# Kernel tuning notes

Measured on AMD Instinct MI355X. Metric: run time of the kernel, lower is better.

Reference implementation:

```python
import jax, jax.numpy as jnp
import numpy as np

B, N, DIM = 8, 512, 512
HEADS, HD = 8, 64          # head_dim = dim // num_heads
E_ATT = 24                 # num_attn_experts, top-k = HEADS
E_FFD, K_FFD = 16, 2       # num_ffd_experts, top-k = ffd_heads
HID = 1024                 # int(dim*mlp_ratio) // ffd_heads = 2048 // 2
TASKS = 9
SWITCH_W, Z_W = 0.01, 0.001
SCALE = HD ** -0.5


def layer_norm(x, g, b, eps=1e-5):
    m = x.mean(-1, keepdims=True)
    v = ((x - m) ** 2).mean(-1, keepdims=True)
    return (x - m) * jax.lax.rsqrt(v + eps) * g + b


def top_k_gating(xf, w_gate, k, n_experts):
    # xf: [T, C], w_gate: [C, E]  (eval mode: no noise)
    logits = xf @ w_gate                                      # [T, E]
    probs = jax.nn.softmax(logits, axis=-1)
    vals, idx = jax.lax.top_k(probs, k)                       # [T, k]
    denom = jax.lax.stop_gradient(vals.sum(-1, keepdims=True) + 1e-6)
    gates = vals / denom                                      # renormalized top-k gates
    one_hot = jax.nn.one_hot(idx, n_experts, dtype=probs.dtype)  # [T, k, E]
    freqs = jax.lax.stop_gradient(one_hot.sum((0, 1)))        # tokens per expert [E]
    p_sum = probs.sum(0)
    switch = n_experts * jnp.sum((p_sum / p_sum.sum()) * (freqs / freqs.sum()))
    z = jnp.mean(jax.nn.logsumexp(logits, axis=-1) ** 2)
    loss = SWITCH_W * switch + Z_W * z
    return gates, one_hot, loss


def _forward(x, task_bh, norm1_g, norm1_b, gate_att, wq, wo_att, kv_w, kv_b,
             norm2_g, norm2_b, gate_mlp, wi, bi, wo_mlp, bo):
    Bs, Ns, C = x.shape
    T = Bs * Ns
    # ---- MoE task attention (MoA-style: experts produce query heads) ----
    x1 = layer_norm(x, norm1_g, norm1_b).reshape(T, C)
    gates, oh, loss1 = top_k_gating(x1, gate_att[task_bh], HEADS, E_ATT)
    # map: per-slot expert query projection (not gate-weighted)
    q_all = jnp.einsum('tc,ech->teh', x1, wq)                 # [T, E, hd]
    q = jnp.einsum('teh,tke->tkh', q_all, oh)                 # [T, H, hd]
    q = q.reshape(Bs, Ns, HEADS, HD)
    kv = x1 @ kv_w + kv_b                                     # shared single-head k,v
    k_, v_ = jnp.split(kv.reshape(Bs, Ns, 2 * HD), 2, axis=-1)
    attn = jnp.einsum('bihd,bjd->bhij', q, k_) * SCALE
    attn = jax.nn.softmax(attn, axis=-1)
    o = jnp.einsum('bhij,bjd->bihd', attn, v_).reshape(T, HEADS, HD)
    # reduce: gate-weighted per-expert output projection
    comb = jnp.einsum('tkd,tk,tke->ted', o, gates, oh)        # [T, E, hd]
    y = jnp.einsum('ted,edc->tc', comb, wo_att).reshape(Bs, Ns, C)
    x = x + y
    # ---- MoE task MLP ----
    x2 = layer_norm(x, norm2_g, norm2_b).reshape(T, C)
    gates2, oh2, loss2 = top_k_gating(x2, gate_mlp[task_bh], K_FFD, E_FFD)
    g_dense = jnp.einsum('tk,tke->te', gates2, oh2)           # sparse gates densified [T,E]
    h = jax.nn.gelu(jnp.einsum('tc,ech->teh', x2, wi) + bi, approximate=False)
    y2 = jnp.einsum('teh,te,ehc->tc', h, g_dense, wo_mlp) + g_dense @ bo
    x = x + y2.reshape(Bs, Ns, C)
    return x, loss1 + loss2


def setup_inputs() -> dict:
    key = jax.random.key(0)
    ks = jax.random.split(key, 8)
    s = 0.02
    return {
        'x': jax.random.normal(ks[0], (B, N, DIM), jnp.float32),
        'task_bh': 3,
        'norm1_g': jnp.ones((DIM,), jnp.float32),
        'norm1_b': jnp.zeros((DIM,), jnp.float32),
        'gate_att': jax.random.normal(ks[1], (TASKS, DIM, E_ATT), jnp.float32) * s,
        'wq': jax.random.normal(ks[2], (E_ATT, DIM, HD), jnp.float32) * s,
        'wo_att': jax.random.normal(ks[3], (E_ATT, HD, DIM), jnp.float32) * s,
        'kv_w': jax.random.normal(ks[4], (DIM, 2 * HD), jnp.float32) * s,
        'kv_b': jnp.zeros((2 * HD,), jnp.float32),
        'norm2_g': jnp.ones((DIM,), jnp.float32),
        'norm2_b': jnp.zeros((DIM,), jnp.float32),
        'gate_mlp': jax.random.normal(ks[5], (TASKS, DIM, E_FFD), jnp.float32) * s,
        'wi': jax.random.normal(ks[6], (E_FFD, DIM, HID), jnp.float32) * s,
        'bi': jnp.zeros((E_FFD, HID), jnp.float32),
        'wo_mlp': jax.random.normal(ks[7], (E_FFD, HID, DIM), jnp.float32) * s,
        'bo': jnp.zeros((E_FFD, DIM), jnp.float32),
    }


def reference(x, task_bh, norm1_g, norm1_b, gate_att, wq, wo_att, kv_w, kv_b,
              norm2_g, norm2_b, gate_mlp, wi, bi, wo_mlp, bo):
    return _forward(x, task_bh, norm1_g, norm1_b, gate_att, wq, wo_att, kv_w, kv_b,
                    norm2_g, norm2_b, gate_mlp, wi, bi, wo_mlp, bo)
```

## Files before the change

### kernel.cpp

```cpp
#include <hip/hip_runtime.h>
#include <math.h>

namespace {

constexpr int T   = 4096;
constexpr int C   = 512;
constexpr int NB  = 8;
constexpr int NS  = 512;
constexpr int HD  = 64;
constexpr int KA  = 8;
constexpr int EA  = 24;
constexpr int EF  = 16;
constexpr int KF  = 2;
constexpr int HID = 1024;

typedef __attribute__((ext_vector_type(8))) short bf16x8;
typedef __attribute__((ext_vector_type(4))) float f32x4;

__device__ inline unsigned short f2bf(float f) {
  unsigned u = __float_as_uint(f);
  return (unsigned short)((u + 0x7FFFu + ((u >> 16) & 1u)) >> 16);
}
__device__ inline float bf2f(unsigned short u) {
  return __uint_as_float((unsigned)u << 16);
}

template <int E, int TS>
__device__ inline bool tile_from_counts(const int* counts, int tile, int& e_out, int& t0_out) {
  int e = 0;
  for (; e < E; e++) {
    int nt = (counts[e] + TS - 1) / TS;
    if (tile < nt) break;
    tile -= nt;
  }
  e_out = e; t0_out = tile * TS;
  return e < E;
}

template <int E, int K, bool RESID>
__global__ __launch_bounds__(1024) void ln_gate_kernel(
    const float* __restrict__ in, const unsigned short* __restrict__ yslot,
    float* __restrict__ resid_out,
    const float* __restrict__ g, const float* __restrict__ b,
    const float* __restrict__ gate_all, const int* __restrict__ task,
    unsigned short* __restrict__ outb,
    float* __restrict__ probs, float* __restrict__ lse_out,
    float* __restrict__ gates, int* __restrict__ idxs) {
  constexpr int TPB = 16;
  constexpr int XSS = 516;
  int tid = threadIdx.x, lane = tid & 63, wv = tid >> 6;
  int tb = blockIdx.x * TPB;
  __shared__ float xs[TPB][XSS];
  __shared__ float lp[2][TPB][E];
  __shared__ __align__(16) float Wt[E][XSS];
  const float* W = gate_all + (size_t)task[0] * C * E;
  for (int i = tid; i < C * E; i += 1024) {
    int c = i / E, e = i - c * E;
    Wt[e][c] = W[i];
  }
  int c0 = lane * 8;
  const float4 g0 = *(const float4*)&g[c0], g1 = *(const float4*)&g[c0 + 4];
  const float4 b0 = *(const float4*)&b[c0], b1 = *(const float4*)&b[c0 + 4];
  {
    int tt = wv;
    int t = tb + tt;
    const float* row = in + (size_t)t * C + c0;
    float4 v0 = *(const float4*)&row[0];
    float4 v1 = *(const float4*)&row[4];
    if (RESID) {
      #pragma unroll
      for (int k = 0; k < KA; k++) {
        uint4 u = *(const uint4*)&yslot[((size_t)t * KA + k) * C + c0];
        const unsigned short* us = (const unsigned short*)&u;
        v0.x += bf2f(us[0]); v0.y += bf2f(us[1]); v0.z += bf2f(us[2]); v0.w += bf2f(us[3]);
        v1.x += bf2f(us[4]); v1.y += bf2f(us[5]); v1.z += bf2f(us[6]); v1.w += bf2f(us[7]);
      }
      *(float4*)&resid_out[(size_t)t * C + c0]     = v0;
      *(float4*)&resid_out[(size_t)t * C + c0 + 4] = v1;
    }
    float s = (v0.x + v0.y) + (v0.z + v0.w) + (v1.x + v1.y) + (v1.z + v1.w);
    #pragma unroll
    for (int m = 1; m < 64; m <<= 1) s += __shfl_xor(s, m);
    float mean = s * (1.f / C);
    float d[8] = {v0.x - mean, v0.y - mean, v0.z - mean, v0.w - mean,
                  v1.x - mean, v1.y - mean, v1.z - mean, v1.w - mean};
    float vv = 0.f;
    #pragma unroll
    for (int j = 0; j < 8; j++) vv += d[j] * d[j];
    #pragma unroll
    for (int m = 1; m < 64; m <<= 1) vv += __shfl_xor(vv, m);
    float r = rsqrtf(vv * (1.f / C) + 1e-5f);
    float o[8];
    o[0] = d[0] * r * g0.x + b0.x; o[1] = d[1] * r * g0.y + b0.y;
    o[2] = d[2] * r * g0.z + b0.z; o[3] = d[3] * r * g0.w + b0.w;
    o[4] = d[4] * r * g1.x + b1.x; o[5] = d[5] * r * g1.y + b1.y;
    o[6] = d[6] * r * g1.z + b1.z; o[7] = d[7] * r * g1.w + b1.w;
    *(ushort4*)&outb[(size_t)t * C + c0] =
        make_ushort4(f2bf(o[0]), f2bf(o[1]), f2bf(o[2]), f2bf(o[3]));
    *(ushort4*)&outb[(size_t)t * C + c0 + 4] =
        make_ushort4(f2bf(o[4]), f2bf(o[5]), f2bf(o[6]), f2bf(o[7]));
    #pragma unroll
    for (int j = 0; j < 8; j++) xs[tt][c0 + j] = o[j];
  }
  __syncthreads();
  if (tid < TPB * E * 2) {
    int half = tid / (TPB * E);
    int rem = tid - half * (TPB * E);
    int e = rem % E, tt = rem / E;
    int cb = half * (C / 2);
    float a0 = 0.f, a1 = 0.f, a2 = 0.f, a3 = 0.f;
    float a4 = 0.f, a5 = 0.f, a6 = 0.f, a7 = 0.f;
    #pragma unroll 4
    for (int c = cb; c < cb + C / 2; c += 8) {
      const float4 xv0 = *(const float4*)&xs[tt][c];
      const float4 xv1 = *(const float4*)&xs[tt][c + 4];
      const float4 wv0 = *(const float4*)&Wt[e][c];
      const float4 wv1 = *(const float4*)&Wt[e][c + 4];
      a0 += xv0.x * wv0.x; a1 += xv0.y * wv0.y;
      a2 += xv0.z * wv0.z; a3 += xv0.w * wv0.w;
      a4 += xv1.x * wv1.x; a5 += xv1.y * wv1.y;
      a6 += xv1.z * wv1.z; a7 += xv1.w * wv1.w;
    }
    lp[half][tt][e] = ((a0 + a1) + (a2 + a3)) + ((a4 + a5) + (a6 + a7));
  }
  __syncthreads();
  {
    int tt = wv;
    int t = tb + tt;
    float lgv = (lane < E) ? (lp[0][tt][lane] + lp[1][tt][lane]) : -3.0e38f;
    float mx = lgv;
    #pragma unroll
    for (int m = 1; m < 64; m <<= 1) mx = fmaxf(mx, __shfl_xor(mx, m));
    float pe = (lane < E) ? expf(lgv - mx) : 0.f;
    float sum = pe;
    #pragma unroll
    for (int m = 1; m < 64; m <<= 1) sum += __shfl_xor(sum, m);
    float inv = 1.f / sum;
    float prob = pe * inv;
    if (lane < E) probs[(size_t)t * E + lane] = prob;
    if (lane == 0) lse_out[t] = mx + logf(sum);
    float pv = (lane < E) ? prob : -1.f;
    float gsum = 0.f, myv = 0.f; int myi = 0;
    for (int k = 0; k < K; k++) {
      float bv = pv; int bi_ = lane;
      #pragma unroll
      for (int m = 1; m < 64; m <<= 1) {
        float ov = __shfl_xor(bv, m); int oi = __shfl_xor(bi_, m);
        if (ov > bv || (ov == bv && oi < bi_)) { bv = ov; bi_ = oi; }
      }
      gsum += bv;
      if (lane == k) { myv = bv; myi = bi_; }
      if (lane == bi_) pv = -1.f;
    }
    if (lane < K) {
      float ginv = 1.f / (gsum + 1e-6f);
      gates[(size_t)t * K + lane] = myv * ginv;
      idxs[(size_t)t * K + lane]  = myi;
    }
  }
}

template <int E>
__global__ __launch_bounds__(512) void bucket_kernel(const int* __restrict__ idx, int nslots,
                                                     int stride, int* counts, int* bucket) {
  __shared__ int lcount[E];
  __shared__ int lbase[E];
  int tid = threadIdx.x;
  if (tid < E) lcount[tid] = 0;
  __syncthreads();
  int s = blockIdx.x * 512 + tid;
  int e = 0, lpos = 0;
  bool valid = (s < nslots);
  if (valid) {
    e = idx[s];
    lpos = atomicAdd(&lcount[e], 1);
  }
  __syncthreads();
  if (tid < E) lbase[tid] = lcount[tid] ? atomicAdd(&counts[tid], lcount[tid]) : 0;
  __syncthreads();
  if (valid) bucket[(size_t)e * stride + lbase[e] + lpos] = s;
}

__global__ __launch_bounds__(256) void tcvt_all(
    const float* __restrict__ wq, const float* __restrict__ wo_a,
    const float* __restrict__ wi, const float* __restrict__ wo_m,
    const float* __restrict__ kvw,
    unsigned short* __restrict__ wqt, unsigned short* __restrict__ woat,
    unsigned short* __restrict__ wit, unsigned short* __restrict__ womt,
    unsigned short* __restrict__ kvwt) {
  int bid = blockIdx.x;
  const float* src; unsigned short* dst; int K, N, nx, rem;
  if (bid < 768)        { src = wq;   dst = wqt;  K = 512;  N = 64;   nx = 2;  rem = bid; }
  else if (bid < 1536)  { src = wo_a; dst = woat; K = 64;   N = 512;  nx = 16; rem = bid - 768; }
  else if (bid < 9728)  { src = wi;   dst = wit;  K = 512;  N = 1024; nx = 32; rem = bid - 1536; }
  else if (bid < 17920) { src = wo_m; dst = womt; K = 1024; N = 512;  nx = 16; rem = bid - 9728; }
  else                  { src = kvw;  dst = kvwt; K = 512;  N = 128;  nx = 4;  rem = bid - 17920; }
  int per = nx * (K / 32);
  int e = rem / per, r2 = rem % per;
  int kt = (r2 / nx) * 32, nt = (r2 % nx) * 32;
  __shared__ float tile[32][33];
  int tid = threadIdx.x;
  const float* S = src + (size_t)e * K * N;
  for (int i = tid; i < 32 * 32; i += 256) {
    int r = i >> 5, c = i & 31;
    tile[r][c] = S[(size_t)(kt + r) * N + nt + c];
  }
  __syncthreads();
  unsigned short* D = dst + (size_t)e * K * N;
  for (int i = tid; i < 32 * 8; i += 256) {
    int n = i >> 3, k4 = (i & 7) * 4;
    ushort4 v;
    v.x = f2bf(tile[k4 + 0][n]); v.y = f2bf(tile[k4 + 1][n]);
    v.z = f2bf(tile[k4 + 2][n]); v.w = f2bf(tile[k4 + 3][n]);
    *(ushort4*)&D[(size_t)(nt + n) * K + kt + k4] = v;
  }
}

__global__ __launch_bounds__(256) void qgemm_mfma(
    const unsigned short* __restrict__ xb, const unsigned short* __restrict__ wqt,
    const int* __restrict__ bucket, const int* __restrict__ counts,
    unsigned short* __restrict__ qb) {
  __shared__ int se, st0;
  int tid = threadIdx.x;
  if (tid == 0) {
    int e, t0;
    bool ok = tile_from_counts<EA, 64>(counts, blockIdx.y, e, t0);
    se = ok ? e : -1; st0 = t0;
  }
  __syncthreads();
  if (se < 0) return;
  int e = se, t0 = st0;
  int cnt = counts[e];
  __shared__ int slots[64];
  __shared__ __align__(16) unsigned short Xb[64][72];
  __shared__ __align__(16) unsigned short Wb[64][72];
  if (tid < 64) {
    int ii = t0 + tid;
    slots[tid] = (ii < cnt) ? bucket[(size_t)e * (T * KA) + ii] : -1;
  }
  __syncthreads();
  int lane = tid & 63, w = tid >> 6;
  int lr = lane & 15, lk = (lane >> 4) * 8, rowq = (lane >> 4) * 4;
  f32x4 acc[4] = {};
  for (int kc = 0; kc < C; kc += 64) {
    __syncthreads();
    #pragma unroll
    for (int it = 0; it < 2; ++it) {
      int i = it * 256 + tid;
      int r = i >> 3, c8 = (i & 7) * 8;
      int s = slots[r];
      uint4 v = make_uint4(0u, 0u, 0u, 0u);
      if (s >= 0) v = *(const uint4*)&xb[(size_t)(s >> 3) * C + kc + c8];
      *(uint4*)&Xb[r][c8] = v;
    }
    #pragma unroll
    for (int it = 0; it < 2; ++it) {
      int i = it * 256 + tid;
      int r = i >> 3, c8 = (i & 7) * 8;
      *(uint4*)&Wb[r][c8] = *(const uint4*)&wqt[((size_t)e * HD + r) * C + kc + c8];
    }
    __syncthreads();
    #pragma unroll
    for (int kk = 0; kk < 64; kk += 32) {
      bf16x8 a = *(const bf16x8*)&Wb[w * 16 + lr][kk + lk];
      #pragma unroll
      for (int mf = 0; mf < 4; mf++) {
        bf16x8 b = *(const bf16x8*)&Xb[mf * 16 + lr][kk + lk];
        acc[mf] = __builtin_amdgcn_mfma_f32_16x16x32_bf16(a, b, acc[mf], 0, 0, 0);
      }
    }
  }
  #pragma unroll
  for (int mf = 0; mf < 4; mf++) {
    int s = slots[mf * 16 + lr];
    if (s < 0) continue;
    ushort4 v = make_ushort4(f2bf(0.125f * acc[mf][0]), f2bf(0.125f * acc[mf][1]),
                             f2bf(0.125f * acc[mf][2]), f2bf(0.125f * acc[mf][3]));
    *(ushort4*)&qb[(size_t)s * HD + w * 16 + rowq] = v;
  }
}

__global__ __launch_bounds__(256) void kv_mfma(
    const unsigned short* __restrict__ xb, const unsigned short* __restrict__ kvwt,
    const float* __restrict__ kvb, unsigned short* __restrict__ Kb,
    unsigned short* __restrict__ Vt) {
  int t0 = blockIdx.x * 16;
  int tid = threadIdx.x;
  __shared__ __align__(16) unsigned short Xs[16][72];
  __shared__ __align__(16) unsigned short Ws[128][72];
  int lane = tid & 63, w = tid >> 6;
  int lr = lane & 15, lk = (lane >> 4) * 8, rowq = (lane >> 4) * 4;
  f32x4 acc[2] = {};
  for (int kc = 0; kc < C; kc += 64) {
    __syncthreads();
    if (tid < 128) {
      int r = tid >> 3, c8 = (tid & 7) * 8;
      *(uint4*)&Xs[r][c8] = *(const uint4*)&xb[(size_t)(t0 + r) * C + kc + c8];
    }
    #pragma unroll
    for (int it = 0; it < 4; ++it) {
      int i = it * 256 + tid;
      int r = i >> 3, c8 = (i & 7) * 8;
      *(uint4*)&Ws[r][c8] = *(const uint4*)&kvwt[(size_t)r * C + kc + c8];
    }
    __syncthreads();
    #pragma unroll
    for (int kk = 0; kk < 64; kk += 32) {
      bf16x8 xf = *(const bf16x8*)&Xs[lr][kk + lk];
      #pragma unroll
      for (int cf = 0; cf < 2; cf++) {
        bf16x8 wf = *(const bf16x8*)&Ws[w * 32 + cf * 16 + lr][kk + lk];
        acc[cf] = __builtin_amdgcn_mfma_f32_16x16x32_bf16(wf, xf, acc[cf], 0, 0, 0);
      }
    }
  }
  int t = t0 + lr;
  int bb = t >> 9, n = t & (NS - 1);
  #pragma unroll
  for (int cf = 0; cf < 2; cf++) {
    #pragma unroll
    for (int r2 = 0; r2 < 4; r2++) {
      int c = w * 32 + cf * 16 + rowq + r2;
      float v = acc[cf][r2] + kvb[c];
      if (c < HD) Kb[(size_t)t * HD + c] = f2bf(v);
      else        Vt[((size_t)bb * HD + (c - HD)) * NS + n] = f2bf(v);
    }
  }
}

__global__ __launch_bounds__(256) void attn_mfma(
    const unsigned short* __restrict__ qb, const unsigned short* __restrict__ Kb,
    const unsigned short* __restrict__ Vt, unsigned short* __restrict__ ob) {
  int qt = blockIdx.x, h = blockIdx.y, b = blockIdx.z;
  int tid = threadIdx.x;
  __shared__ __align__(16) unsigned short Qs[64][72];
  __shared__ __align__(16) unsigned short Ks[64][72];
  __shared__ __align__(16) unsigned short Vs[64][72];
  __shared__ __align__(16) unsigned short Ps[64][72];
  int i0 = qt * 64;
  #pragma unroll
  for (int it = 0; it < 2; ++it) {
    int i = it * 256 + tid;
    int r = i >> 3, c8 = (i & 7) * 8;
    *(uint4*)&Qs[r][c8] = *(const uint4*)&qb[(((size_t)(b * NS + i0 + r)) * KA + h) * HD + c8];
  }
  int lane = tid & 63, w = tid >> 6;
  int lr = lane & 15, lk = (lane >> 4) * 8, rowq = (lane >> 4) * 4;
  f32x4 acc_o[4] = {};
  float m_run = -3.0e38f, l_run = 0.f;
  for (int jt = 0; jt < NS / 64; ++jt) {
    __syncthreads();
    #pragma unroll
    for (int it = 0; it < 2; ++it) {
      int i = it * 256 + tid;
      int r = i >> 3, c8 = (i & 7) * 8;
      *(uint4*)&Ks[r][c8] = *(const uint4*)&Kb[((size_t)(b * NS + jt * 64 + r)) * HD + c8];
      *(uint4*)&Vs[r][c8] = *(const uint4*)&Vt[((size_t)b * HD + r) * NS + jt * 64 + c8];
    }
    __syncthreads();
    f32x4 acc_s[4] = {};
    #pragma unroll
    for (int kk = 0; kk < 64; kk += 32) {
      bf16x8 qf = *(const bf16x8*)&Qs[w * 16 + lr][kk + lk];
      #pragma unroll
      for (int kf = 0; kf < 4; kf++) {
        bf16x8 kr = *(const bf16x8*)&Ks[kf * 16 + lr][kk + lk];
        acc_s[kf] = __builtin_amdgcn_mfma_f32_16x16x32_bf16(kr, qf, acc_s[kf], 0, 0, 0);
      }
    }
    float pmax = acc_s[0][0];
    #pragma unroll
    for (int kf = 0; kf < 4; kf++)
      #pragma unroll
      for (int r = 0; r < 4; r++) pmax = fmaxf(pmax, acc_s[kf][r]);
    pmax = fmaxf(pmax, __shfl_xor(pmax, 16));
    pmax = fmaxf(pmax, __shfl_xor(pmax, 32));
    float m_new = fmaxf(m_run, pmax);
    float scl = expf(m_run - m_new);
    float rs = 0.f;
    #pragma unroll
    for (int kf = 0; kf < 4; kf++)
      #pragma unroll
      for (int r = 0; r < 4; r++) {
        float pv = expf(acc_s[kf][r] - m_new);
        rs += pv;
        Ps[w * 16 + lr][kf * 16 + rowq + r] = f2bf(pv);
      }
    rs += __shfl_xor(rs, 16);
    rs += __shfl_xor(rs, 32);
    l_run = l_run * scl + rs;
    m_run = m_new;
    __syncthreads();
    #pragma unroll
    for (int df = 0; df < 4; df++) {
      acc_o[df][0] *= scl; acc_o[df][1] *= scl;
      acc_o[df][2] *= scl; acc_o[df][3] *= scl;
    }
    #pragma unroll
    for (int kk = 0; kk < 64; kk += 32) {
      bf16x8 pf = *(const bf16x8*)&Ps[w * 16 + lr][kk + lk];
      #pragma unroll
      for (int df = 0; df < 4; df++) {
        bf16x8 vf = *(const bf16x8*)&Vs[df * 16 + lr][kk + lk];
        acc_o[df] = __builtin_amdgcn_mfma_f32_16x16x32_bf16(vf, pf, acc_o[df], 0, 0, 0);
      }
    }
  }
  float inv = 1.f / l_run;
  int token = b * NS + i0 + w * 16 + lr;
  #pragma unroll
  for (int df = 0; df < 4; df++) {
    ushort4 v = make_ushort4(f2bf(acc_o[df][0] * inv), f2bf(acc_o[df][1] * inv),
                             f2bf(acc_o[df][2] * inv), f2bf(acc_o[df][3] * inv));
    *(ushort4*)&ob[((size_t)token * KA + h) * HD + df * 16 + rowq] = v;
  }
}

__global__ __launch_bounds__(256) void oproj_mfma(
    const unsigned short* __restrict__ ob, const unsigned short* __restrict__ wot,
    const float* __restrict__ gates, const int* __restrict__ bucket,
    const int* __restrict__ counts, unsigned short* __restrict__ y_slot) {
  __shared__ int se, st0;
  int tid = threadIdx.x;
  if (tid == 0) {
    int e, t0;
    bool ok = tile_from_counts<EA, 128>(counts, blockIdx.y, e, t0);
    se = ok ? e : -1; st0 = t0;
  }
  __syncthreads();
  if (se < 0) return;
  int e = se, t0 = st0;
  int c0 = blockIdx.x * 128;
  int cnt = counts[e];
  __shared__ int slots[128];
  __shared__ float gs[128];
  __shared__ __align__(16) unsigned short Xb[128][72];
  __shared__ __align__(16) unsigned short Wb[128][72];
  if (tid < 128) {
    int ii = t0 + tid;
    int s = (ii < cnt) ? bucket[(size_t)e * (T * KA) + ii] : -1;
    slots[tid] = s;
    gs[tid] = (s >= 0) ? gates[s] : 0.f;
  }
  __syncthreads();
  #pragma unroll
  for (int it = 0; it < 4; ++it) {
    int i = it * 256 + tid;
    int r = i >> 3, c8 = (i & 7) * 8;
    int s = slots[r];
    uint4 vo = make_uint4(0u, 0u, 0u, 0u);
    if (s >= 0) {
      float g = gs[r];
      uint4 u = *(const uint4*)&ob[(size_t)s * HD + c8];
      const unsigned short* us = (const unsigned short*)&u;
      unsigned short* vs = (unsigned short*)&vo;
      #pragma unroll
      for (int k = 0; k < 8; k++) vs[k] = f2bf(g * bf2f(us[k]));
    }
    *(uint4*)&Xb[r][c8] = vo;
  }
  #pragma unroll
  for (int it = 0; it < 4; ++it) {
    int i = it * 256 + tid;
    int r = i >> 3, c8 = (i & 7) * 8;
    *(uint4*)&Wb[r][c8] = *(const uint4*)&wot[((size_t)e * C + c0 + r) * HD + c8];
  }
  __syncthreads();
  int lane = tid & 63, wid = tid >> 6;
  int wr = wid & 1, wc = wid >> 1;
  int lr = lane & 15, lk = (lane >> 4) * 8, rowq = (lane >> 4) * 4;
  f32x4 acc[4][4] = {};
  #pragma unroll
  for (int kk = 0; kk < 64; kk += 32) {
    bf16x8 a[4], b[4];
    #pragma unroll
    for (int nf = 0; nf < 4; nf++) a[nf] = *(const bf16x8*)&Wb[wc * 64 + nf * 16 + lr][kk + lk];
    #pragma unroll
    for (int mf = 0; mf < 4; mf++) b[mf] = *(const bf16x8*)&Xb[wr * 64 + mf * 16 + lr][kk + lk];
    #pragma unroll
    for (int nf = 0; nf < 4; nf++)
      #pragma unroll
      for (int mf = 0; mf < 4; mf++)
        acc[nf][mf] = __builtin_amdgcn_mfma_f32_16x16x32_bf16(a[nf], b[mf], acc[nf][mf], 0, 0, 0);
  }
  #pragma unroll
  for (int mf = 0; mf < 4; mf++) {
    int si = wr * 64 + mf * 16 + lr;
    int s = slots[si];
    if (s < 0) continue;
    size_t base = (size_t)s * C + c0 + wc * 64;
    #pragma unroll
    for (int nf = 0; nf < 4; nf++) {
      ushort4 v = make_ushort4(f2bf(acc[nf][mf][0]), f2bf(acc[nf][mf][1]),
                               f2bf(acc[nf][mf][2]), f2bf(acc[nf][mf][3]));
      *(ushort4*)&y_slot[base + nf * 16 + rowq] = v;
    }
  }
}

__global__ __launch_bounds__(256) void mlp1_mfma(
    const unsigned short* __restrict__ xb, const unsigned short* __restrict__ wit,
    const float* __restrict__ bi, const int* __restrict__ bucket,
    const int* __restrict__ counts, unsigned short* __restrict__ h) {
  __shared__ int se, st0;
  int tid = threadIdx.x;
  if (tid == 0) {
    int e, t0;
    bool ok = tile_from_counts<EF, 64>(counts, blockIdx.y, e, t0);
    se = ok ? e : -1; st0 = t0;
  }
  __syncthreads();
  if (se < 0) return;
  int e = se, t0 = st0;
  int j0 = blockIdx.x * 64;
  int cnt = counts[e];
  __shared__ int slots[64];
  __shared__ __align__(16) unsigned short Xb[64][72];
  __shared__ __align__(16) unsigned short Wb[64][72];
  if (tid < 64) {
    int ii = t0 + tid;
    slots[tid] = (ii < cnt) ? bucket[(size_t)e * (T * KF) + ii] : -1;
  }
  __syncthreads();
  int lane = tid & 63, w = tid >> 6;
  int lr = lane & 15, lk = (lane >> 4) * 8, rowq = (lane >> 4) * 4;
  f32x4 acc[4] = {};
  for (int kc = 0; kc < C; kc += 64) {
    __syncthreads();
    #pragma unroll
    for (int it = 0; it < 2; ++it) {
      int i = it * 256 + tid;
      int r = i >> 3, c8 = (i & 7) * 8;
      int s = slots[r];
      uint4 v = make_uint4(0u, 0u, 0u, 0u);
      if (s >= 0) v = *(const uint4*)&xb[(size_t)(s >> 1) * C + kc + c8];
      *(uint4*)&Xb[r][c8] = v;
    }
    #pragma unroll
    for (int it = 0; it < 2; ++it) {
      int i = it * 256 + tid;
      int r = i >> 3, c8 = (i & 7) * 8;
      *(uint4*)&Wb[r][c8] = *(const uint4*)&wit[((size_t)e * HID + j0 + r) * C + kc + c8];
    }
    __syncthreads();
    #pragma unroll
    for (int kk = 0; kk < 64; kk += 32) {
      bf16x8 a = *(const bf16x8*)&Wb[w * 16 + lr][kk + lk];
      #pragma unroll
      for (int mf = 0; mf < 4; mf++) {
        bf16x8 b = *(const bf16x8*)&Xb[mf * 16 + lr][kk + lk];
        acc[mf] = __builtin_amdgcn_mfma_f32_16x16x32_bf16(a, b, acc[mf], 0, 0, 0);
      }
    }
  }
  #pragma unroll
  for (int mf = 0; mf < 4; mf++) {
    int s = slots[mf * 16 + lr];
    if (s < 0) continue;
    int j = j0 + w * 16 + rowq;
    const float4 b4 = *(const float4*)&bi[(size_t)e * HID + j];
    float v0 = acc[mf][0] + b4.x, v1 = acc[mf][1] + b4.y;
    float v2 = acc[mf][2] + b4.z, v3 = acc[mf][3] + b4.w;
    v0 = 0.5f * v0 * (1.f + erff(v0 * 0.70710678118654752f));
    v1 = 0.5f * v1 * (1.f + erff(v1 * 0.70710678118654752f));
    v2 = 0.5f * v2 * (1.f + erff(v2 * 0.70710678118654752f));
    v3 = 0.5f * v3 * (1.f + erff(v3 * 0.70710678118654752f));
    *(ushort4*)&h[(size_t)s * HID + j] = make_ushort4(f2bf(v0), f2bf(v1), f2bf(v2), f2bf(v3));
  }
}

__global__ __launch_bounds__(256) void mlp2_mfma(
    const unsigned short* __restrict__ h, const unsigned short* __restrict__ wot,
    const float* __restrict__ bo, const float* __restrict__ gates2,
    const int* __restrict__ bucket, const int* __restrict__ counts,
    unsigned short* __restrict__ y2) {
  __shared__ int se, st0;
  int tid = threadIdx.x;
  if (tid == 0) {
    int e, t0;
    bool ok = tile_from_counts<EF, 64>(counts, blockIdx.y, e, t0);
    se = ok ? e : -1; st0 = t0;
  }
  __syncthreads();
  if (se < 0) return;
  int e = se, t0 = st0;
  int c0 = blockIdx.x * 64;
  int cnt = counts[e];
  __shared__ int slots[64];
  __shared__ __align__(16) unsigned short Xb[64][72];
  __shared__ __align__(16) unsigned short Wb[64][72];
  if (tid < 64) {
    int ii = t0 + tid;
    slots[tid] = (ii < cnt) ? bucket[(size_t)e * (T * KF) + ii] : -1;
  }
  __syncthreads();
  int lane = tid & 63, w = tid >> 6;
  int lr = lane & 15, lk = (lane >> 4) * 8, rowq = (lane >> 4) * 4;
  f32x4 acc[4] = {};
  for (int kc = 0; kc < HID; kc += 64) {
    __syncthreads();
    #pragma unroll
    for (int it = 0; it < 2; ++it) {
      int i = it * 256 + tid;
      int r = i >> 3, c8 = (i & 7) * 8;
      int s = slots[r];
      uint4 v = make_uint4(0u, 0u, 0u, 0u);
      if (s >= 0) v = *(const uint4*)&h[(size_t)s * HID + kc + c8];
      *(uint4*)&Xb[r][c8] = v;
    }
    #pragma unroll
    for (int it = 0; it < 2; ++it) {
      int i = it * 256 + tid;
      int r = i >> 3, c8 = (i & 7) * 8;
      *(uint4*)&Wb[r][c8] = *(const uint4*)&wot[((size_t)e * C + c0 + r) * HID + kc + c8];
    }
    __syncthreads();
    #pragma unroll
    for (int kk = 0; kk < 64; kk += 32) {
      bf16x8 a = *(const bf16x8*)&Wb[w * 16 + lr][kk + lk];
      #pragma unroll
      for (int mf = 0; mf < 4; mf++) {
        bf16x8 b = *(const bf16x8*)&Xb[mf * 16 + lr][kk + lk];
        acc[mf] = __builtin_amdgcn_mfma_f32_16x16x32_bf16(a, b, acc[mf], 0, 0, 0);
      }
    }
  }
  #pragma unroll
  for (int mf = 0; mf < 4; mf++) {
    int s = slots[mf * 16 + lr];
    if (s < 0) continue;
    float g = gates2[s];
    int cc = c0 + w * 16 + rowq;
    const float4 b4 = *(const float4*)&bo[(size_t)e * C + cc];
    ushort4 v = make_ushort4(f2bf(g * (acc[mf][0] + b4.x)),
                             f2bf(g * (acc[mf][1] + b4.y)),
                             f2bf(g * (acc[mf][2] + b4.z)),
                             f2bf(g * (acc[mf][3] + b4.w)));
    *(ushort4*)&y2[(size_t)s * C + cc] = v;
  }
}

__global__ void final_kernel(const unsigned short* __restrict__ y2, float* __restrict__ xout) {
  int t = blockIdx.x, tid = threadIdx.x;
  int c = tid * 2;
  unsigned u0 = *(const unsigned*)&y2[(size_t)(t * 2) * C + c];
  unsigned u1 = *(const unsigned*)&y2[(size_t)(t * 2 + 1) * C + c];
  xout[(size_t)t * C + c]     += bf2f((unsigned short)(u0 & 0xFFFF)) + bf2f((unsigned short)(u1 & 0xFFFF));
  xout[(size_t)t * C + c + 1] += bf2f((unsigned short)(u0 >> 16)) + bf2f((unsigned short)(u1 >> 16));
}

__global__ __launch_bounds__(256) void reduce_gating_all(
    const float* __restrict__ probs1, const float* __restrict__ lse1,
    const int* __restrict__ idx1,
    const float* __restrict__ probs2, const float* __restrict__ lse2,
    const int* __restrict__ idx2, float* __restrict__ accum) {
  constexpr int TPB = 64, TPW = 16;
  int which = blockIdx.y;
  int E = which ? EF : EA;
  int K = which ? KF : KA;
  const float* probs = which ? probs2 : probs1;
  const float* lse   = which ? lse2 : lse1;
  const int* idxs    = which ? idx2 : idx1;
  float* psum = accum + (which ? 49 : 0);
  float* freq = accum + (which ? 65 : 24);
  float* zsum = accum + (which ? 81 : 48);
  int tid = threadIdx.x, lane = tid & 63, wv = tid >> 6;
  int t0 = blockIdx.x * TPB + wv * TPW;
  float ps = 0.f, fr = 0.f;
  if (lane < E) {
    for (int i = 0; i < TPW; i++) {
      int t = t0 + i;
      ps += probs[(size_t)t * E + lane];
      for (int k = 0; k < K; k++)
        fr += (idxs[(size_t)t * K + k] == lane) ? 1.f : 0.f;
    }
  }
  float z = 0.f;
  for (int i = lane; i < TPW; i += 64) {
    float l = lse[t0 + i];
    z += l * l;
  }
  #pragma unroll
  for (int m = 1; m < 64; m <<= 1) z += __shfl_xor(z, m);
  __shared__ float sps[4][EA];
  __shared__ float sfr[4][EA];
  __shared__ float sz[4];
  if (lane < E) { sps[wv][lane] = ps; sfr[wv][lane] = fr; }
  if (lane == 0) sz[wv] = z;
  __syncthreads();
  if (tid < E) {
    atomicAdd(&psum[tid], sps[0][tid] + sps[1][tid] + sps[2][tid] + sps[3][tid]);
    atomicAdd(&freq[tid], sfr[0][tid] + sfr[1][tid] + sfr[2][tid] + sfr[3][tid]);
  }
  if (tid == 255) atomicAdd(zsum, sz[0] + sz[1] + sz[2] + sz[3]);
}

__global__ void loss_kernel(const float* __restrict__ acc, float* __restrict__ out) {
  const float* p1 = acc;      const float* f1 = acc + 24; float z1 = acc[48];
  const float* p2 = acc + 49; const float* f2 = acc + 65; float z2 = acc[81];
  float sp1 = 0.f, sf1 = 0.f;
  for (int e = 0; e < 24; e++) { sp1 += p1[e]; sf1 += f1[e]; }
  float sw1 = 0.f;
  for (int e = 0; e < 24; e++) sw1 += (p1[e] / sp1) * (f1[e] / sf1);
  sw1 *= 24.f;
  float sp2 = 0.f, sf2 = 0.f;
  for (int e = 0; e < 16; e++) { sp2 += p2[e]; sf2 += f2[e]; }
  float sw2 = 0.f;
  for (int e = 0; e < 16; e++) sw2 += (p2[e] / sp2) * (f2[e] / sf2);
  sw2 *= 16.f;
  out[0] = 0.01f * sw1 + 0.001f * (z1 / T) + 0.01f * sw2 + 0.001f * (z2 / T);
}

}

extern "C" void kernel_launch(void* const* d_in, const int* in_sizes, int n_in,
                              void* d_out, int out_size, void* d_ws, size_t ws_size,
                              hipStream_t stream) {
  const float* x      = (const float*)d_in[0];
  const int*   task   = (const int*)d_in[1];
  const float* n1g    = (const float*)d_in[2];
  const float* n1b    = (const float*)d_in[3];
  const float* gate_a = (const float*)d_in[4];
  const float* wq     = (const float*)d_in[5];
  const float* wo_a   = (const float*)d_in[6];
  const float* kvw    = (const float*)d_in[7];
  const float* kvb    = (const float*)d_in[8];
  const float* n2g    = (const float*)d_in[9];
  const float* n2b    = (const float*)d_in[10];
  const float* gate_m = (const float*)d_in[11];
  const float* wi     = (const float*)d_in[12];
  const float* bi     = (const float*)d_in[13];
  const float* wo_m   = (const float*)d_in[14];
  const float* bo     = (const float*)d_in[15];
  float* out = (float*)d_out;

  char* p = (char*)d_ws;
  unsigned short* x1b = (unsigned short*)p; p += (size_t)T * C * 2;
  unsigned short* qb = (unsigned short*)p;  p += (size_t)T * KA * HD * 2;
  unsigned short* ob = (unsigned short*)p;  p += (size_t)T * KA * HD * 2;
  unsigned short* Kb = (unsigned short*)p;  p += (size_t)T * HD * 2;
  unsigned short* Vt = (unsigned short*)p;  p += (size_t)T * HD * 2;
  char* un = p;                      p += (size_t)T * KA * C * 2;
  unsigned short* y_slot  = (unsigned short*)un;
  unsigned short* h       = (unsigned short*)un;
  unsigned short* y2_slot = (unsigned short*)(un + (size_t)T * KF * HID * 2);
  unsigned short* wqt = (unsigned short*)p;  p += (size_t)EA * C * HD * 2;
  unsigned short* woat = (unsigned short*)p; p += (size_t)EA * HD * C * 2;
  unsigned short* wit = (unsigned short*)p;  p += (size_t)EF * C * HID * 2;
  unsigned short* womt = (unsigned short*)p; p += (size_t)EF * HID * C * 2;
  unsigned short* kvwt = (unsigned short*)p; p += (size_t)(2 * HD) * C * 2;
  float* probs1 = (float*)p;         p += (size_t)T * EA * 4;
  float* lse1 = (float*)p;           p += (size_t)T * 4;
  float* gates1 = (float*)p;         p += (size_t)T * KA * 4;
  int* idx1 = (int*)p;               p += (size_t)T * KA * 4;
  float* probs2 = (float*)p;         p += (size_t)T * EF * 4;
  float* lse2 = (float*)p;           p += (size_t)T * 4;
  float* gates2 = (float*)p;         p += (size_t)T * KF * 4;
  int* idx2 = (int*)p;               p += (size_t)T * KF * 4;
  int* bucket_a = (int*)p;           p += (size_t)EA * (T * KA) * 4;
  int* bucket_f = (int*)p;           p += (size_t)EF * (T * KF) * 4;
  int* counts_a = (int*)p;           p += 32 * 4;
  int* counts_f = (int*)p;           p += 32 * 4;
  float* accum = (float*)p;          p += 128 * 4;

  hipMemsetAsync(counts_a, 0, (32 + 32 + 128) * 4, stream);

  tcvt_all<<<17984, 256, 0, stream>>>(wq, wo_a, wi, wo_m, kvw, wqt, woat, wit, womt, kvwt);

  ln_gate_kernel<EA, KA, false><<<T / 16, 1024, 0, stream>>>(
      x, y_slot, out, n1g, n1b, gate_a, task, x1b, probs1, lse1, gates1, idx1);
  bucket_kernel<EA><<<(T * KA + 511) / 512, 512, 0, stream>>>(idx1, T * KA, T * KA,
                                                              counts_a, bucket_a);
  qgemm_mfma<<<dim3(1, 536), 256, 0, stream>>>(x1b, wqt, bucket_a, counts_a, qb);
  kv_mfma<<<T / 16, 256, 0, stream>>>(x1b, kvwt, kvb, Kb, Vt);
  attn_mfma<<<dim3(NS / 64, KA, NB), 256, 0, stream>>>(qb, Kb, Vt, ob);
  oproj_mfma<<<dim3(4, 280), 256, 0, stream>>>(ob, woat, gates1, bucket_a, counts_a, y_slot);
  ln_gate_kernel<EF, KF, true><<<T / 16, 1024, 0, stream>>>(
      x, y_slot, out, n2g, n2b, gate_m, task, x1b, probs2, lse2, gates2, idx2);
  bucket_kernel<EF><<<(T * KF + 511) / 512, 512, 0, stream>>>(idx2, T * KF, T * KF,
                                                              counts_f, bucket_f);
  mlp1_mfma<<<dim3(16, 144), 256, 0, stream>>>(x1b, wit, bi, bucket_f, counts_f, h);
  mlp2_mfma<<<dim3(8, 144), 256, 0, stream>>>(h, womt, bo, gates2, bucket_f, counts_f, y2_slot);
  final_kernel<<<T, 256, 0, stream>>>(y2_slot, out);
  reduce_gating_all<<<dim3(T / 64, 2), 256, 0, stream>>>(probs1, lse1, idx1,
                                                         probs2, lse2, idx2, accum);
  loss_kernel<<<1, 1, 0, stream>>>(accum, out + (size_t)T * C);
}
```

Baseline: 229.4 us.

## Merge Q and KV projections into one launch, retile weight convert and attention

Combines the routed Q projection and the shared KV projection into a single kernel whose grid covers both kinds of tile, saving one launch and letting the two overlap. The weight convert-transpose kernel now uses 64x64 tiles with float4 loads, giving four times fewer blocks, though its stores become scalar 2-byte writes. Attention blocks drop to 128 threads covering 32 query rows each, which doubles the block count to raise occupancy but loads each K/V tile twice as often overall.

```diff
diff --git a/kernel.cpp b/kernel.cpp
--- a/kernel.cpp
+++ b/kernel.cpp
@@ -190,157 +190,153 @@
     unsigned short* __restrict__ kvwt) {
   int bid = blockIdx.x;
   const float* src; unsigned short* dst; int K, N, nx, rem;
-  if (bid < 768)        { src = wq;   dst = wqt;  K = 512;  N = 64;   nx = 2;  rem = bid; }
-  else if (bid < 1536)  { src = wo_a; dst = woat; K = 64;   N = 512;  nx = 16; rem = bid - 768; }
-  else if (bid < 9728)  { src = wi;   dst = wit;  K = 512;  N = 1024; nx = 32; rem = bid - 1536; }
-  else if (bid < 17920) { src = wo_m; dst = womt; K = 1024; N = 512;  nx = 16; rem = bid - 9728; }
-  else                  { src = kvw;  dst = kvwt; K = 512;  N = 128;  nx = 4;  rem = bid - 17920; }
-  int per = nx * (K / 32);
+  if (bid < 192)       { src = wq;   dst = wqt;  K = 512;  N = 64;   nx = 1;  rem = bid; }
+  else if (bid < 384)  { src = wo_a; dst = woat; K = 64;   N = 512;  nx = 8;  rem = bid - 192; }
+  else if (bid < 2432) { src = wi;   dst = wit;  K = 512;  N = 1024; nx = 16; rem = bid - 384; }
+  else if (bid < 4480) { src = wo_m; dst = womt; K = 1024; N = 512;  nx = 8;  rem = bid - 2432; }
+  else                 { src = kvw;  dst = kvwt; K = 512;  N = 128;  nx = 2;  rem = bid - 4480; }
+  int per = nx * (K / 64);
   int e = rem / per, r2 = rem % per;
-  int kt = (r2 / nx) * 32, nt = (r2 % nx) * 32;
-  __shared__ float tile[32][33];
+  int kt = (r2 / nx) * 64, nt = (r2 % nx) * 64;
+  __shared__ float tile[64][65];
   int tid = threadIdx.x;
   const float* S = src + (size_t)e * K * N;
-  for (int i = tid; i < 32 * 32; i += 256) {
-    int r = i >> 5, c = i & 31;
-    tile[r][c] = S[(size_t)(kt + r) * N + nt + c];
+  for (int i = tid; i < 64 * 16; i += 256) {
+    int r = i >> 4, c4 = (i & 15) * 4;
+    const float4 v = *(const float4*)&S[(size_t)(kt + r) * N + nt + c4];
+    tile[r][c4 + 0] = v.x; tile[r][c4 + 1] = v.y;
+    tile[r][c4 + 2] = v.z; tile[r][c4 + 3] = v.w;
   }
   __syncthreads();
   unsigned short* D = dst + (size_t)e * K * N;
-  for (int i = tid; i < 32 * 8; i += 256) {
-    int n = i >> 3, k4 = (i & 7) * 4;
-    ushort4 v;
-    v.x = f2bf(tile[k4 + 0][n]); v.y = f2bf(tile[k4 + 1][n]);
-    v.z = f2bf(tile[k4 + 2][n]); v.w = f2bf(tile[k4 + 3][n]);
-    *(ushort4*)&D[(size_t)(nt + n) * K + kt + k4] = v;
-  }
-}
-
-__global__ __launch_bounds__(256) void qgemm_mfma(
+  for (int i = tid; i < 64 * 64; i += 256) {
+    int k = i & 63, n = i >> 6;
+    D[(size_t)(nt + n) * K + kt + k] = f2bf(tile[k][n]);
+  }
+}
+
+__global__ __launch_bounds__(256) void qkv_mfma(
     const unsigned short* __restrict__ xb, const unsigned short* __restrict__ wqt,
+    const unsigned short* __restrict__ kvwt, const float* __restrict__ kvb,
     const int* __restrict__ bucket, const int* __restrict__ counts,
-    unsigned short* __restrict__ qb) {
+    unsigned short* __restrict__ qb, unsigned short* __restrict__ Kb,
+    unsigned short* __restrict__ Vt) {
+  __shared__ __align__(16) unsigned short smem[16 * 72 + 128 * 72];
+  __shared__ int slots[64];
   __shared__ int se, st0;
   int tid = threadIdx.x;
-  if (tid == 0) {
-    int e, t0;
-    bool ok = tile_from_counts<EA, 64>(counts, blockIdx.y, e, t0);
-    se = ok ? e : -1; st0 = t0;
-  }
-  __syncthreads();
-  if (se < 0) return;
-  int e = se, t0 = st0;
-  int cnt = counts[e];
-  __shared__ int slots[64];
-  __shared__ __align__(16) unsigned short Xb[64][72];
-  __shared__ __align__(16) unsigned short Wb[64][72];
-  if (tid < 64) {
-    int ii = t0 + tid;
-    slots[tid] = (ii < cnt) ? bucket[(size_t)e * (T * KA) + ii] : -1;
-  }
-  __syncthreads();
   int lane = tid & 63, w = tid >> 6;
   int lr = lane & 15, lk = (lane >> 4) * 8, rowq = (lane >> 4) * 4;
-  f32x4 acc[4] = {};
-  for (int kc = 0; kc < C; kc += 64) {
-    __syncthreads();
-    #pragma unroll
-    for (int it = 0; it < 2; ++it) {
-      int i = it * 256 + tid;
-      int r = i >> 3, c8 = (i & 7) * 8;
-      int s = slots[r];
-      uint4 v = make_uint4(0u, 0u, 0u, 0u);
-      if (s >= 0) v = *(const uint4*)&xb[(size_t)(s >> 3) * C + kc + c8];
-      *(uint4*)&Xb[r][c8] = v;
-    }
-    #pragma unroll
-    for (int it = 0; it < 2; ++it) {
-      int i = it * 256 + tid;
-      int r = i >> 3, c8 = (i & 7) * 8;
-      *(uint4*)&Wb[r][c8] = *(const uint4*)&wqt[((size_t)e * HD + r) * C + kc + c8];
-    }
-    __syncthreads();
-    #pragma unroll
-    for (int kk = 0; kk < 64; kk += 32) {
-      bf16x8 a = *(const bf16x8*)&Wb[w * 16 + lr][kk + lk];
-      #pragma unroll
-      for (int mf = 0; mf < 4; mf++) {
-        bf16x8 b = *(const bf16x8*)&Xb[mf * 16 + lr][kk + lk];
-        acc[mf] = __builtin_amdgcn_mfma_f32_16x16x32_bf16(a, b, acc[mf], 0, 0, 0);
-      }
-    }
-  }
-  #pragma unroll
-  for (int mf = 0; mf < 4; mf++) {
-    int s = slots[mf * 16 + lr];
-    if (s < 0) continue;
-    ushort4 v = make_ushort4(f2bf(0.125f * acc[mf][0]), f2bf(0.125f * acc[mf][1]),
-                             f2bf(0.125f * acc[mf][2]), f2bf(0.125f * acc[mf][3]));
-    *(ushort4*)&qb[(size_t)s * HD + w * 16 + rowq] = v;
-  }
-}
-
-__global__ __launch_bounds__(256) void kv_mfma(
-    const unsigned short* __restrict__ xb, const unsigned short* __restrict__ kvwt,
-    const float* __restrict__ kvb, unsigned short* __restrict__ Kb,
-    unsigned short* __restrict__ Vt) {
-  int t0 = blockIdx.x * 16;
-  int tid = threadIdx.x;
-  __shared__ __align__(16) unsigned short Xs[16][72];
-  __shared__ __align__(16) unsigned short Ws[128][72];
-  int lane = tid & 63, w = tid >> 6;
-  int lr = lane & 15, lk = (lane >> 4) * 8, rowq = (lane >> 4) * 4;
-  f32x4 acc[2] = {};
-  for (int kc = 0; kc < C; kc += 64) {
-    __syncthreads();
-    if (tid < 128) {
-      int r = tid >> 3, c8 = (tid & 7) * 8;
-      *(uint4*)&Xs[r][c8] = *(const uint4*)&xb[(size_t)(t0 + r) * C + kc + c8];
-    }
-    #pragma unroll
-    for (int it = 0; it < 4; ++it) {
-      int i = it * 256 + tid;
-      int r = i >> 3, c8 = (i & 7) * 8;
-      *(uint4*)&Ws[r][c8] = *(const uint4*)&kvwt[(size_t)r * C + kc + c8];
-    }
-    __syncthreads();
-    #pragma unroll
-    for (int kk = 0; kk < 64; kk += 32) {
-      bf16x8 xf = *(const bf16x8*)&Xs[lr][kk + lk];
-      #pragma unroll
-      for (int cf = 0; cf < 2; cf++) {
-        bf16x8 wf = *(const bf16x8*)&Ws[w * 32 + cf * 16 + lr][kk + lk];
-        acc[cf] = __builtin_amdgcn_mfma_f32_16x16x32_bf16(wf, xf, acc[cf], 0, 0, 0);
-      }
-    }
-  }
-  int t = t0 + lr;
-  int bb = t >> 9, n = t & (NS - 1);
-  #pragma unroll
-  for (int cf = 0; cf < 2; cf++) {
-    #pragma unroll
-    for (int r2 = 0; r2 < 4; r2++) {
-      int c = w * 32 + cf * 16 + rowq + r2;
-      float v = acc[cf][r2] + kvb[c];
-      if (c < HD) Kb[(size_t)t * HD + c] = f2bf(v);
-      else        Vt[((size_t)bb * HD + (c - HD)) * NS + n] = f2bf(v);
-    }
-  }
-}
-
-__global__ __launch_bounds__(256) void attn_mfma(
+  if ((int)blockIdx.y < T / 16) {
+    int t0 = blockIdx.y * 16;
+    unsigned short* Xs = smem;
+    unsigned short* Ws = smem + 16 * 72;
+    f32x4 acc[2] = {};
+    for (int kc = 0; kc < C; kc += 64) {
+      __syncthreads();
+      if (tid < 128) {
+        int r = tid >> 3, c8 = (tid & 7) * 8;
+        *(uint4*)&Xs[r * 72 + c8] = *(const uint4*)&xb[(size_t)(t0 + r) * C + kc + c8];
+      }
+      #pragma unroll
+      for (int it = 0; it < 4; ++it) {
+        int i = it * 256 + tid;
+        int r = i >> 3, c8 = (i & 7) * 8;
+        *(uint4*)&Ws[r * 72 + c8] = *(const uint4*)&kvwt[(size_t)r * C + kc + c8];
+      }
+      __syncthreads();
+      #pragma unroll
+      for (int kk = 0; kk < 64; kk += 32) {
+        bf16x8 xf = *(const bf16x8*)&Xs[lr * 72 + kk + lk];
+        #pragma unroll
+        for (int cf = 0; cf < 2; cf++) {
+          bf16x8 wf = *(const bf16x8*)&Ws[(w * 32 + cf * 16 + lr) * 72 + kk + lk];
+          acc[cf] = __builtin_amdgcn_mfma_f32_16x16x32_bf16(wf, xf, acc[cf], 0, 0, 0);
+        }
+      }
+    }
+    int t = t0 + lr;
+    int bb = t >> 9, n = t & (NS - 1);
+    #pragma unroll
+    for (int cf = 0; cf < 2; cf++) {
+      #pragma unroll
+      for (int r2 = 0; r2 < 4; r2++) {
+        int c = w * 32 + cf * 16 + rowq + r2;
+        float v = acc[cf][r2] + kvb[c];
+        if (c < HD) Kb[(size_t)t * HD + c] = f2bf(v);
+        else        Vt[((size_t)bb * HD + (c - HD)) * NS + n] = f2bf(v);
+      }
+    }
+  } else {
+    if (tid == 0) {
+      int e, t0;
+      bool ok = tile_from_counts<EA, 64>(counts, blockIdx.y - T / 16, e, t0);
+      se = ok ? e : -1; st0 = t0;
+    }
+    __syncthreads();
+    if (se < 0) return;
+    int e = se, t0 = st0;
+    int cnt = counts[e];
+    unsigned short* Xb = smem;
+    unsigned short* Wb = smem + 64 * 72;
+    if (tid < 64) {
+      int ii = t0 + tid;
+      slots[tid] = (ii < cnt) ? bucket[(size_t)e * (T * KA) + ii] : -1;
+    }
+    __syncthreads();
+    f32x4 acc[4] = {};
+    for (int kc = 0; kc < C; kc += 64) {
+      __syncthreads();
+      #pragma unroll
+      for (int it = 0; it < 2; ++it) {
+        int i = it * 256 + tid;
+        int r = i >> 3, c8 = (i & 7) * 8;
+        int s = slots[r];
+        uint4 v = make_uint4(0u, 0u, 0u, 0u);
+        if (s >= 0) v = *(const uint4*)&xb[(size_t)(s >> 3) * C + kc + c8];
+        *(uint4*)&Xb[r * 72 + c8] = v;
+      }
+      #pragma unroll
+      for (int it = 0; it < 2; ++it) {
+        int i = it * 256 + tid;
+        int r = i >> 3, c8 = (i & 7) * 8;
+        *(uint4*)&Wb[r * 72 + c8] = *(const uint4*)&wqt[((size_t)e * HD + r) * C + kc + c8];
+      }
+      __syncthreads();
+      #pragma unroll
+      for (int kk = 0; kk < 64; kk += 32) {
+        bf16x8 a = *(const bf16x8*)&Wb[(w * 16 + lr) * 72 + kk + lk];
+        #pragma unroll
+        for (int mf = 0; mf < 4; mf++) {
+          bf16x8 b = *(const bf16x8*)&Xb[(mf * 16 + lr) * 72 + kk + lk];
+          acc[mf] = __builtin_amdgcn_mfma_f32_16x16x32_bf16(a, b, acc[mf], 0, 0, 0);
+        }
+      }
+    }
+    #pragma unroll
+    for (int mf = 0; mf < 4; mf++) {
+      int s = slots[mf * 16 + lr];
+      if (s < 0) continue;
+      ushort4 v = make_ushort4(f2bf(0.125f * acc[mf][0]), f2bf(0.125f * acc[mf][1]),
+                               f2bf(0.125f * acc[mf][2]), f2bf(0.125f * acc[mf][3]));
+      *(ushort4*)&qb[(size_t)s * HD + w * 16 + rowq] = v;
+    }
+  }
+}
+
+__global__ __launch_bounds__(128) void attn_mfma(
     const unsigned short* __restrict__ qb, const unsigned short* __restrict__ Kb,
     const unsigned short* __restrict__ Vt, unsigned short* __restrict__ ob) {
   int qt = blockIdx.x, h = blockIdx.y, b = blockIdx.z;
   int tid = threadIdx.x;
-  __shared__ __align__(16) unsigned short Qs[64][72];
+  __shared__ __align__(16) unsigned short Qs[32][72];
   __shared__ __align__(16) unsigned short Ks[64][72];
   __shared__ __align__(16) unsigned short Vs[64][72];
-  __shared__ __align__(16) unsigned short Ps[64][72];
-  int i0 = qt * 64;
+  __shared__ __align__(16) unsigned short Ps[32][72];
+  int i0 = qt * 32;
   #pragma unroll
   for (int it = 0; it < 2; ++it) {
-    int i = it * 256 + tid;
+    int i = it * 128 + tid;
     int r = i >> 3, c8 = (i & 7) * 8;
     *(uint4*)&Qs[r][c8] = *(const uint4*)&qb[(((size_t)(b * NS + i0 + r)) * KA + h) * HD + c8];
   }
@@ -351,8 +347,8 @@
   for (int jt = 0; jt < NS / 64; ++jt) {
     __syncthreads();
     #pragma unroll
-    for (int it = 0; it < 2; ++it) {
-      int i = it * 256 + tid;
+    for (int it = 0; it < 4; ++it) {
+      int i = it * 128 + tid;
       int r = i >> 3, c8 = (i & 7) * 8;
       *(uint4*)&Ks[r][c8] = *(const uint4*)&Kb[((size_t)(b * NS + jt * 64 + r)) * HD + c8];
       *(uint4*)&Vs[r][c8] = *(const uint4*)&Vt[((size_t)b * HD + r) * NS + jt * 64 + c8];
@@ -765,15 +761,15 @@
 
   hipMemsetAsync(counts_a, 0, (32 + 32 + 128) * 4, stream);
 
-  tcvt_all<<<17984, 256, 0, stream>>>(wq, wo_a, wi, wo_m, kvw, wqt, woat, wit, womt, kvwt);
+  tcvt_all<<<4496, 256, 0, stream>>>(wq, wo_a, wi, wo_m, kvw, wqt, woat, wit, womt, kvwt);
 
   ln_gate_kernel<EA, KA, false><<<T / 16, 1024, 0, stream>>>(
       x, y_slot, out, n1g, n1b, gate_a, task, x1b, probs1, lse1, gates1, idx1);
   bucket_kernel<EA><<<(T * KA + 511) / 512, 512, 0, stream>>>(idx1, T * KA, T * KA,
                                                               counts_a, bucket_a);
-  qgemm_mfma<<<dim3(1, 536), 256, 0, stream>>>(x1b, wqt, bucket_a, counts_a, qb);
-  kv_mfma<<<T / 16, 256, 0, stream>>>(x1b, kvwt, kvb, Kb, Vt);
-  attn_mfma<<<dim3(NS / 64, KA, NB), 256, 0, stream>>>(qb, Kb, Vt, ob);
+  qkv_mfma<<<dim3(1, T / 16 + 536), 256, 0, stream>>>(x1b, wqt, kvwt, kvb,
+                                                      bucket_a, counts_a, qb, Kb, Vt);
+  attn_mfma<<<dim3(NS / 32, KA, NB), 128, 0, stream>>>(qb, Kb, Vt, ob);
   oproj_mfma<<<dim3(4, 280), 256, 0, stream>>>(ob, woat, gates1, bucket_a, counts_a, y_slot);
   ln_gate_kernel<EF, KF, true><<<T / 16, 1024, 0, stream>>>(
       x, y_slot, out, n2g, n2b, gate_m, task, x1b, probs2, lse2, gates2, idx2);
```

Measured after the change: 216.3 us. 1.06x faster.
